# Kernel optimization log

Hardware: AMD Instinct MI355X
Metric: run time of the kernel (lower is better)

The kernel has to match this reference:

```python
import jax, jax.numpy as jnp
import numpy as np

DIM = 4096
N_HEADS = 32
HEAD_DIM = DIM // N_HEADS
BATCH = 2
SEQ = 1024
THETA = 10000.0
NEG_INF = -1e9


def _rope_cos_sin(seq_len, head_dim):
    # NOTE: original code constructs RotatePosEmbedding with config.dim but applies
    # it per-head; the only shape-consistent interpretation (standard Llama RoPE)
    # uses head_dim frequencies, which is what we implement.
    inv_freq = 1.0 / (THETA ** (jnp.arange(0, head_dim, 2, dtype=jnp.float32) / head_dim))
    angles = jnp.arange(seq_len, dtype=jnp.float32)[:, None] * inv_freq[None, :]  # [S, hd/2]
    return jnp.cos(angles), jnp.sin(angles)


def _apply_rope(x, cos, sin):
    # x: [B,S,H,hd]; rotate consecutive pairs (complex multiply)
    B, S, H, hd = x.shape
    xr = x.reshape(B, S, H, hd // 2, 2)
    x0, x1 = xr[..., 0], xr[..., 1]
    c = cos[None, :, None, :]
    s = sin[None, :, None, :]
    out = jnp.stack([x0 * c - x1 * s, x0 * s + x1 * c], axis=-1)
    return out.reshape(B, S, H, hd)


def setup_inputs() -> dict:
    key = jax.random.key(0)
    ks = jax.random.split(key, 9)
    x = jax.random.normal(ks[0], (BATCH, SEQ, DIM), dtype=jnp.float32)
    scale = 1.0 / np.sqrt(DIM)
    wq = jax.random.normal(ks[1], (DIM, DIM), dtype=jnp.float32) * scale
    wk = jax.random.normal(ks[2], (DIM, DIM), dtype=jnp.float32) * scale
    wv = jax.random.normal(ks[3], (DIM, DIM), dtype=jnp.float32) * scale
    wo = jax.random.normal(ks[4], (DIM, DIM), dtype=jnp.float32) * scale
    bq = jax.random.normal(ks[5], (DIM,), dtype=jnp.float32) * 0.01
    bk = jax.random.normal(ks[6], (DIM,), dtype=jnp.float32) * 0.01
    bv = jax.random.normal(ks[7], (DIM,), dtype=jnp.float32) * 0.01
    bo = jax.random.normal(ks[8], (DIM,), dtype=jnp.float32) * 0.01
    # causal additive mask [S,S]
    mask = jnp.where(jnp.tril(jnp.ones((SEQ, SEQ), dtype=bool)), 0.0, NEG_INF).astype(jnp.float32)
    return {"x": x, "wq": wq, "bq": bq, "wk": wk, "bk": bk, "wv": wv, "bv": bv,
            "wo": wo, "bo": bo, "mask": mask, "start_pos": 0}


def reference(x, wq, bq, wk, bk, wv, bv, wo, bo, mask, start_pos):
    B, S, D = x.shape
    H, hd = N_HEADS, D // N_HEADS
    q = (x @ wq.T + bq).reshape(B, S, H, hd)
    k = (x @ wk.T + bk).reshape(B, S, H, hd)
    v = (x @ wv.T + bv).reshape(B, S, H, hd)
    cos, sin = _rope_cos_sin(S, hd)
    q = _apply_rope(q, cos, sin)
    k = _apply_rope(k, cos, sin)
    # start_pos == 0 prefill: cache slice [:start_pos+S] equals current k/v
    scores = jnp.einsum('bqhd,bkhd->bhqk', q, k) / np.sqrt(hd).astype(np.float32)
    scores = scores + mask[None, None, :, :]
    attn = jax.nn.softmax(scores, axis=-1)
    out = jnp.einsum('bhqk,bkhd->bqhd', attn, v).reshape(B, S, D)
    return out @ wo.T + bo
```

## Files before the change

### kernel.cpp

```cpp
#include <hip/hip_runtime.h>
#include <hip/hip_bf16.h>

#define DIM   4096
#define NH    32
#define HD    128
#define BATCH 2
#define SEQ   1024
#define MROWS (BATCH*SEQ)

typedef __attribute__((ext_vector_type(8))) short bf16x8;
typedef __attribute__((ext_vector_type(4))) short s16x4;
typedef __attribute__((ext_vector_type(4))) float f32x4;

__device__ inline void gload_lds16(const void* g, void* l) {
  __builtin_amdgcn_global_load_lds(
      (const __attribute__((address_space(1))) void*)g,
      (__attribute__((address_space(3))) void*)l, 16, 0, 0);
}

__device__ inline float bf2f(short b) {
  unsigned u = ((unsigned)(unsigned short)b) << 16;
  return __uint_as_float(u);
}
__device__ inline unsigned short f2bfu(float f) {
  __hip_bfloat16 h = __float2bfloat16(f);
  return *reinterpret_cast<unsigned short*>(&h);
}

__global__ void cvt_bf16_kernel(const float* __restrict__ in,
                                unsigned short* __restrict__ out, long n4) {
  long i = blockIdx.x * (long)blockDim.x + threadIdx.x;
  long stride = (long)gridDim.x * blockDim.x;
  for (; i < n4; i += stride) {
    float4 v = ((const float4*)in)[i];
    ushort4 o;
    o.x = f2bfu(v.x); o.y = f2bfu(v.y); o.z = f2bfu(v.z); o.w = f2bfu(v.w);
    ((ushort4*)out)[i] = o;
  }
}

__global__ void rope_table_kernel(float* __restrict__ cosT, float* __restrict__ sinT) {
  int s = blockIdx.x;
  int p = threadIdx.x;
  float inv = powf(10000.0f, -((float)(2 * p)) / 128.0f);
  float a = (float)s * inv;
  cosT[s * 64 + p] = cosf(a);
  sinT[s * 64 + p] = sinf(a);
}

__global__ void rope_apply_kernel(unsigned short* __restrict__ t,
                                  const float* __restrict__ cosT,
                                  const float* __restrict__ sinT) {
  int c = blockIdx.x * blockDim.x + threadIdx.x;
  long e = (long)c * 8;
  int row = (int)(e >> 12);
  int col = (int)(e & (DIM - 1));
  int s = row & (SEQ - 1);
  int d = col & (HD - 1);
  int p0 = d >> 1;
  bf16x8 v = *(bf16x8*)&t[e];
  f32x4 cv = *(const f32x4*)&cosT[s * 64 + p0];
  f32x4 sv = *(const f32x4*)&sinT[s * 64 + p0];
  bf16x8 o;
#pragma unroll
  for (int j = 0; j < 4; ++j) {
    float x0 = bf2f(v[2 * j]);
    float x1 = bf2f(v[2 * j + 1]);
    o[2 * j]     = (short)f2bfu(x0 * cv[j] - x1 * sv[j]);
    o[2 * j + 1] = (short)f2bfu(x0 * sv[j] + x1 * cv[j]);
  }
  *(bf16x8*)&t[e] = o;
}

template <typename OutT>
__global__ __launch_bounds__(256) void gemm_bt_kernel(
    const unsigned short* __restrict__ A, const unsigned short* __restrict__ Bw,
    const float* __restrict__ bias, OutT* __restrict__ C, int M, int N, int K) {
  __shared__ unsigned short As[128 * 32];
  __shared__ unsigned short Bs[128 * 32];
  const int t = threadIdx.x;
  const int lane = t & 63;
  const int w = t >> 6;
  const int wr = w >> 1, wc = w & 1;
  const int m0 = blockIdx.y * 128;
  const int n0 = blockIdx.x * 128;

  const int ar0 = t >> 2;
  const int acol = (t & 3) * 8;
  const unsigned short* Ag0 = A + (size_t)(m0 + ar0) * K + acol;
  const unsigned short* Ag1 = A + (size_t)(m0 + 64 + ar0) * K + acol;
  const unsigned short* Bg0 = Bw + (size_t)(n0 + ar0) * K + acol;
  const unsigned short* Bg1 = Bw + (size_t)(n0 + 64 + ar0) * K + acol;
  unsigned short* Al0 = &As[(size_t)t * 8];
  unsigned short* Al1 = &As[(size_t)(256 + t) * 8];
  unsigned short* Bl0 = &Bs[(size_t)t * 8];
  unsigned short* Bl1 = &Bs[(size_t)(256 + t) * 8];

  f32x4 acc[4][4] = {};

  const int aro = wr * 64 + (lane & 15);
  const int bro = wc * 64 + (lane & 15);
  const int ko = (lane >> 4) * 8;

  for (int k0 = 0; k0 < K; k0 += 32) {
    gload_lds16(Ag0 + k0, Al0);
    gload_lds16(Ag1 + k0, Al1);
    gload_lds16(Bg0 + k0, Bl0);
    gload_lds16(Bg1 + k0, Bl1);
    __syncthreads();
    bf16x8 af[4], bfr[4];
#pragma unroll
    for (int i = 0; i < 4; ++i)
      af[i] = *(const bf16x8*)&As[(aro + i * 16) * 32 + ko];
#pragma unroll
    for (int j = 0; j < 4; ++j)
      bfr[j] = *(const bf16x8*)&Bs[(bro + j * 16) * 32 + ko];
#pragma unroll
    for (int i = 0; i < 4; ++i)
#pragma unroll
      for (int j = 0; j < 4; ++j)
        acc[i][j] = __builtin_amdgcn_mfma_f32_16x16x32_bf16(af[i], bfr[j], acc[i][j], 0, 0, 0);
    __syncthreads();
  }

  const int mrow = m0 + wr * 64 + (lane >> 4) * 4;
  const int ncol = n0 + wc * 64 + (lane & 15);
#pragma unroll
  for (int j = 0; j < 4; ++j) {
    float bj = bias[ncol + j * 16];
#pragma unroll
    for (int i = 0; i < 4; ++i) {
#pragma unroll
      for (int r = 0; r < 4; ++r) {
        float v = acc[i][j][r] + bj;
        if constexpr (sizeof(OutT) == 2) {
          ((unsigned short*)C)[(size_t)(mrow + i * 16 + r) * N + (ncol + j * 16)] = f2bfu(v);
        } else {
          ((float*)C)[(size_t)(mrow + i * 16 + r) * N + (ncol + j * 16)] = v;
        }
      }
    }
  }
}

__global__ __launch_bounds__(256, 1) void flash_attn_kernel(
    const unsigned short* __restrict__ Q, const unsigned short* __restrict__ Kk,
    const unsigned short* __restrict__ V, unsigned short* __restrict__ O) {
  __shared__ unsigned short Ks[64 * 128];
  __shared__ unsigned short Vt[128 * 64];
  __shared__ unsigned short Ps[4][32 * 64];

  const int p  = blockIdx.x;
  const int bh = blockIdx.y;
  const int b  = bh >> 5;
  const int hh = bh & 31;
  const int t    = threadIdx.x;
  const int lane = t & 63;
  const int w    = t >> 6;
  const int np   = lane & 15;
  const int hq   = lane >> 4;

  const size_t headoff = (size_t)b * SEQ * DIM + (size_t)hh * HD;
  const unsigned short* Qg = Q  + headoff;
  const unsigned short* Kg = Kk + headoff;
  const unsigned short* Vg = V  + headoff;
  unsigned short*       Og = O  + headoff;

  const int krow = t >> 2;
  const int kc0  = (t & 3) * 32;
  const int vr0  = (t & 15) * 4;
  const int vc0  = (t >> 4) * 8;

  unsigned short* Pw = &Ps[w][0];
  const float SCALE = 0.08838834764831843f;

  bf16x8 vk[4], vv[4];

#pragma unroll 1
  for (int pass = 0; pass < 2; ++pass) {
    const int qt    = pass ? (7 - p) : p;
    const int nt    = 2 * qt + 2;
    const int qbase = qt * 128 + w * 32;

    bf16x8 qf[2][4];
#pragma unroll
    for (int rb = 0; rb < 2; ++rb)
#pragma unroll
      for (int kb = 0; kb < 4; ++kb)
        qf[rb][kb] = *(const bf16x8*)&Qg[(size_t)(qbase + rb * 16 + np) * DIM + kb * 32 + hq * 8];

    f32x4 acc[2][8] = {};
    float m_run[2][4], l_run[2][4];
#pragma unroll
    for (int rb = 0; rb < 2; ++rb)
#pragma unroll
      for (int r = 0; r < 4; ++r) { m_run[rb][r] = -3.0e38f; l_run[rb][r] = 0.0f; }

    {
      const unsigned short* kp = Kg + (size_t)krow * DIM + kc0;
      const unsigned short* vp = Vg + (size_t)vr0 * DIM + vc0;
#pragma unroll
      for (int jj = 0; jj < 4; ++jj) vk[jj] = *(const bf16x8*)(kp + jj * 8);
#pragma unroll
      for (int jj = 0; jj < 4; ++jj) vv[jj] = *(const bf16x8*)(vp + (size_t)jj * DIM);
    }

#pragma unroll 1
    for (int kt = 0; kt < nt; ++kt) {
      __syncthreads();

#pragma unroll
      for (int jj = 0; jj < 4; ++jj) {
        int c = (t & 3) * 4 + jj;
        *(bf16x8*)((char*)Ks + krow * 256 + ((c ^ (krow & 7)) << 4)) = vk[jj];
      }
#pragma unroll
      for (int i = 0; i < 8; ++i) {
        int col = vc0 + i;
        s16x4 sv;
        sv[0] = vv[0][i]; sv[1] = vv[1][i]; sv[2] = vv[2][i]; sv[3] = vv[3][i];
        *(s16x4*)((char*)Vt + ((col * 128 + vr0 * 2) ^ ((col & 7) << 4))) = sv;
      }
      __syncthreads();

      if (kt + 1 < nt) {
        const unsigned short* kp = Kg + (size_t)((kt + 1) * 64 + krow) * DIM + kc0;
        const unsigned short* vp = Vg + (size_t)((kt + 1) * 64 + vr0) * DIM + vc0;
#pragma unroll
        for (int jj = 0; jj < 4; ++jj) vk[jj] = *(const bf16x8*)(kp + jj * 8);
#pragma unroll
        for (int jj = 0; jj < 4; ++jj) vv[jj] = *(const bf16x8*)(vp + (size_t)jj * DIM);
      }

      f32x4 sc[4][2] = {};
#pragma unroll
      for (int ct = 0; ct < 4; ++ct) {
#pragma unroll
        for (int kb = 0; kb < 4; ++kb) {
          bf16x8 kf = *(const bf16x8*)((char*)Ks + (ct * 16 + np) * 256 +
                                       (((kb * 4 + hq) ^ (np & 7)) << 4));
          sc[ct][0] = __builtin_amdgcn_mfma_f32_16x16x32_bf16(qf[0][kb], kf, sc[ct][0], 0, 0, 0);
          sc[ct][1] = __builtin_amdgcn_mfma_f32_16x16x32_bf16(qf[1][kb], kf, sc[ct][1], 0, 0, 0);
        }
      }

      const bool maskt = (kt >= 2 * qt);
#pragma unroll
      for (int ct = 0; ct < 4; ++ct) {
        int kvc = kt * 64 + ct * 16 + np;
#pragma unroll
        for (int rb = 0; rb < 2; ++rb)
#pragma unroll
          for (int r = 0; r < 4; ++r) {
            float v = sc[ct][rb][r] * SCALE;
            if (maskt && kvc > qbase + rb * 16 + hq * 4 + r) v = -1.0e9f;
            sc[ct][rb][r] = v;
          }
      }

      float sf[2][4];
#pragma unroll
      for (int rb = 0; rb < 2; ++rb)
#pragma unroll
        for (int r = 0; r < 4; ++r) {
          float tmax = fmaxf(fmaxf(sc[0][rb][r], sc[1][rb][r]),
                             fmaxf(sc[2][rb][r], sc[3][rb][r]));
          tmax = fmaxf(tmax, __shfl_xor(tmax, 1));
          tmax = fmaxf(tmax, __shfl_xor(tmax, 2));
          tmax = fmaxf(tmax, __shfl_xor(tmax, 4));
          tmax = fmaxf(tmax, __shfl_xor(tmax, 8));
          float mn = fmaxf(m_run[rb][r], tmax);
          sf[rb][r] = __expf(m_run[rb][r] - mn);
          m_run[rb][r] = mn;
        }

#pragma unroll
      for (int rb = 0; rb < 2; ++rb)
#pragma unroll
        for (int r = 0; r < 4; ++r) {
          int prow = rb * 16 + hq * 4 + r;
          int swz = (prow & 7) << 4;
          float rsum = 0.f;
#pragma unroll
          for (int ct = 0; ct < 4; ++ct) {
            float pv = __expf(sc[ct][rb][r] - m_run[rb][r]);
            rsum += pv;
            *(unsigned short*)((char*)Pw + ((prow * 128 + (ct * 16 + np) * 2) ^ swz)) = f2bfu(pv);
          }
          rsum += __shfl_xor(rsum, 1);
          rsum += __shfl_xor(rsum, 2);
          rsum += __shfl_xor(rsum, 4);
          rsum += __shfl_xor(rsum, 8);
          l_run[rb][r] = l_run[rb][r] * sf[rb][r] + rsum;
        }

#pragma unroll
      for (int rb = 0; rb < 2; ++rb)
#pragma unroll
        for (int nt2 = 0; nt2 < 8; ++nt2)
#pragma unroll
          for (int r = 0; r < 4; ++r)
            acc[rb][nt2][r] *= sf[rb][r];

#pragma unroll
      for (int kb2 = 0; kb2 < 2; ++kb2) {
        bf16x8 pa0 = *(const bf16x8*)((char*)Pw +
            (((0 * 16 + np) * 128 + kb2 * 64 + hq * 16) ^ ((np & 7) << 4)));
        bf16x8 pa1 = *(const bf16x8*)((char*)Pw +
            (((1 * 16 + np) * 128 + kb2 * 64 + hq * 16) ^ ((np & 7) << 4)));
#pragma unroll
        for (int nt2 = 0; nt2 < 8; ++nt2) {
          int col = nt2 * 16 + np;
          bf16x8 vf = *(const bf16x8*)((char*)Vt +
              ((col * 128 + kb2 * 64 + hq * 16) ^ ((col & 7) << 4)));
          acc[0][nt2] = __builtin_amdgcn_mfma_f32_16x16x32_bf16(pa0, vf, acc[0][nt2], 0, 0, 0);
          acc[1][nt2] = __builtin_amdgcn_mfma_f32_16x16x32_bf16(pa1, vf, acc[1][nt2], 0, 0, 0);
        }
      }
    }

#pragma unroll
    for (int rb = 0; rb < 2; ++rb)
#pragma unroll
      for (int r = 0; r < 4; ++r) {
        float rl = 1.0f / l_run[rb][r];
        int orow = qbase + rb * 16 + hq * 4 + r;
#pragma unroll
        for (int nt2 = 0; nt2 < 8; ++nt2)
          Og[(size_t)orow * DIM + nt2 * 16 + np] = f2bfu(acc[rb][nt2][r] * rl);
      }
  }
}

extern "C" void kernel_launch(void* const* d_in, const int* in_sizes, int n_in,
                              void* d_out, int out_size, void* d_ws, size_t ws_size,
                              hipStream_t stream) {
  const float* x  = (const float*)d_in[0];
  const float* wq = (const float*)d_in[1];
  const float* bq = (const float*)d_in[2];
  const float* wk = (const float*)d_in[3];
  const float* bk = (const float*)d_in[4];
  const float* wv = (const float*)d_in[5];
  const float* bv = (const float*)d_in[6];
  const float* wo = (const float*)d_in[7];
  const float* bo = (const float*)d_in[8];
  float* out = (float*)d_out;

  char* ws = (char*)d_ws;
  unsigned short* xb  = (unsigned short*)(ws);
  unsigned short* wqb = (unsigned short*)(ws + (16ll  << 20));
  unsigned short* wkb = (unsigned short*)(ws + (48ll  << 20));
  unsigned short* wvb = (unsigned short*)(ws + (80ll  << 20));
  unsigned short* wob = (unsigned short*)(ws + (112ll << 20));
  unsigned short* qb  = (unsigned short*)(ws + (144ll << 20));
  unsigned short* kb_ = (unsigned short*)(ws + (160ll << 20));
  unsigned short* vb  = (unsigned short*)(ws + (176ll << 20));
  unsigned short* ab  = (unsigned short*)(ws + (192ll << 20));
  float* cosT = (float*)(ws + (208ll << 20));
  float* sinT = (float*)(ws + (208ll << 20) + (256 << 10));

  cvt_bf16_kernel<<<2048, 256, 0, stream>>>(x,  xb,  (long)MROWS * DIM / 4);
  cvt_bf16_kernel<<<2048, 256, 0, stream>>>(wq, wqb, (long)DIM * DIM / 4);
  cvt_bf16_kernel<<<2048, 256, 0, stream>>>(wk, wkb, (long)DIM * DIM / 4);
  cvt_bf16_kernel<<<2048, 256, 0, stream>>>(wv, wvb, (long)DIM * DIM / 4);
  cvt_bf16_kernel<<<2048, 256, 0, stream>>>(wo, wob, (long)DIM * DIM / 4);

  rope_table_kernel<<<SEQ, 64, 0, stream>>>(cosT, sinT);

  dim3 gg(DIM / 128, MROWS / 128);
  gemm_bt_kernel<unsigned short><<<gg, 256, 0, stream>>>(xb, wqb, bq, qb, MROWS, DIM, DIM);
  gemm_bt_kernel<unsigned short><<<gg, 256, 0, stream>>>(xb, wkb, bk, kb_, MROWS, DIM, DIM);
  gemm_bt_kernel<unsigned short><<<gg, 256, 0, stream>>>(xb, wvb, bv, vb, MROWS, DIM, DIM);

  int rope_blocks = (MROWS * DIM / 8) / 256;
  rope_apply_kernel<<<rope_blocks, 256, 0, stream>>>(qb, cosT, sinT);
  rope_apply_kernel<<<rope_blocks, 256, 0, stream>>>(kb_, cosT, sinT);

  dim3 ga(4, BATCH * NH);
  flash_attn_kernel<<<ga, 256, 0, stream>>>(qb, kb_, vb, ab);

  gemm_bt_kernel<float><<<gg, 256, 0, stream>>>(ab, wob, bo, out, MROWS, DIM, DIM);
}
```

Baseline: 635.2 us.

## Fuse QKV projections into one GEMM with double-buffered 256x128 pipelined tiles

The Q, K and V weights are concatenated into one 12288-wide weight so a single GEMM produces a packed QKV buffer. RoPE then runs once over the Q and K columns, and flash attention reads from the packed layout with a 12288-element row stride. The GEMM kernel is rewritten to use 256x128 tiles with 512 threads, a K step of 64, double-buffered LDS loaded through XOR-swizzled direct-to-LDS copies, and a grouped block remap for cache locality. The aim is fewer launches, better reuse of x across the three projections, and overlap of global loads with MFMA work. In exchange it uses more LDS and registers per block and adds a small bias-concatenation kernel.

Measured after the change: 560.1 us. 11.8% less time.

```diff
diff --git a/kernel.cpp b/kernel.cpp
--- a/kernel.cpp
+++ b/kernel.cpp
@@ -7,6 +7,7 @@
 #define BATCH 2
 #define SEQ   1024
 #define MROWS (BATCH*SEQ)
+#define LDQ   12288
 
 typedef __attribute__((ext_vector_type(8))) short bf16x8;
 typedef __attribute__((ext_vector_type(4))) short s16x4;
@@ -39,6 +40,14 @@
   }
 }
 
+__global__ void concat3_kernel(const float* __restrict__ a, const float* __restrict__ b,
+                               const float* __restrict__ c, float* __restrict__ o) {
+  int i = blockIdx.x * blockDim.x + threadIdx.x;
+  if (i < 4096) o[i] = a[i];
+  else if (i < 8192) o[i] = b[i - 4096];
+  else if (i < 12288) o[i] = c[i - 8192];
+}
+
 __global__ void rope_table_kernel(float* __restrict__ cosT, float* __restrict__ sinT) {
   int s = blockIdx.x;
   int p = threadIdx.x;
@@ -48,17 +57,18 @@
   sinT[s * 64 + p] = sinf(a);
 }
 
-__global__ void rope_apply_kernel(unsigned short* __restrict__ t,
+__global__ void rope_apply_kernel(unsigned short* __restrict__ qkv,
                                   const float* __restrict__ cosT,
                                   const float* __restrict__ sinT) {
   int c = blockIdx.x * blockDim.x + threadIdx.x;
   long e = (long)c * 8;
-  int row = (int)(e >> 12);
-  int col = (int)(e & (DIM - 1));
+  int row = (int)(e >> 13);
+  int col = (int)(e & 8191);
   int s = row & (SEQ - 1);
   int d = col & (HD - 1);
   int p0 = d >> 1;
-  bf16x8 v = *(bf16x8*)&t[e];
+  unsigned short* p = qkv + (size_t)row * LDQ + col;
+  bf16x8 v = *(bf16x8*)p;
   f32x4 cv = *(const f32x4*)&cosT[s * 64 + p0];
   f32x4 sv = *(const f32x4*)&sinT[s * 64 + p0];
   bf16x8 o;
@@ -69,83 +79,121 @@
     o[2 * j]     = (short)f2bfu(x0 * cv[j] - x1 * sv[j]);
     o[2 * j + 1] = (short)f2bfu(x0 * sv[j] + x1 * cv[j]);
   }
-  *(bf16x8*)&t[e] = o;
+  *(bf16x8*)p = o;
+}
+
+__device__ __forceinline__ void stage_tile(
+    const unsigned short* __restrict__ A, const unsigned short* __restrict__ Bw,
+    unsigned short* Asl, unsigned short* Bsl,
+    int m0, int n0, int K, int kbase, int t) {
+#pragma unroll
+  for (int j = 0; j < 4; ++j) {
+    int ci = j * 512 + t;
+    int r = ci >> 3, c = ci & 7;
+    gload_lds16(A + (size_t)(m0 + r) * K + kbase + ((c ^ (r & 7)) << 3), Asl + ci * 8);
+  }
+#pragma unroll
+  for (int j = 0; j < 2; ++j) {
+    int ci = j * 512 + t;
+    int r = ci >> 3, c = ci & 7;
+    gload_lds16(Bw + (size_t)(n0 + r) * K + kbase + ((c ^ (r & 7)) << 3), Bsl + ci * 8);
+  }
 }
 
 template <typename OutT>
-__global__ __launch_bounds__(256) void gemm_bt_kernel(
+__global__ __launch_bounds__(512, 2) void gemm_bt_p_kernel(
     const unsigned short* __restrict__ A, const unsigned short* __restrict__ Bw,
     const float* __restrict__ bias, OutT* __restrict__ C, int M, int N, int K) {
-  __shared__ unsigned short As[128 * 32];
-  __shared__ unsigned short Bs[128 * 32];
+  __shared__ unsigned short As[2][256 * 64];
+  __shared__ unsigned short Bs[2][128 * 64];
   const int t = threadIdx.x;
   const int lane = t & 63;
   const int w = t >> 6;
-  const int wr = w >> 1, wc = w & 1;
-  const int m0 = blockIdx.y * 128;
-  const int n0 = blockIdx.x * 128;
-
-  const int ar0 = t >> 2;
-  const int acol = (t & 3) * 8;
-  const unsigned short* Ag0 = A + (size_t)(m0 + ar0) * K + acol;
-  const unsigned short* Ag1 = A + (size_t)(m0 + 64 + ar0) * K + acol;
-  const unsigned short* Bg0 = Bw + (size_t)(n0 + ar0) * K + acol;
-  const unsigned short* Bg1 = Bw + (size_t)(n0 + 64 + ar0) * K + acol;
-  unsigned short* Al0 = &As[(size_t)t * 8];
-  unsigned short* Al1 = &As[(size_t)(256 + t) * 8];
-  unsigned short* Bl0 = &Bs[(size_t)t * 8];
-  unsigned short* Bl1 = &Bs[(size_t)(256 + t) * 8];
-
-  f32x4 acc[4][4] = {};
-
-  const int aro = wr * 64 + (lane & 15);
-  const int bro = wc * 64 + (lane & 15);
-  const int ko = (lane >> 4) * 8;
-
-  for (int k0 = 0; k0 < K; k0 += 32) {
-    gload_lds16(Ag0 + k0, Al0);
-    gload_lds16(Ag1 + k0, Al1);
-    gload_lds16(Bg0 + k0, Bl0);
-    gload_lds16(Bg1 + k0, Bl1);
-    __syncthreads();
-    bf16x8 af[4], bfr[4];
-#pragma unroll
-    for (int i = 0; i < 4; ++i)
-      af[i] = *(const bf16x8*)&As[(aro + i * 16) * 32 + ko];
-#pragma unroll
-    for (int j = 0; j < 4; ++j)
-      bfr[j] = *(const bf16x8*)&Bs[(bro + j * 16) * 32 + ko];
-#pragma unroll
-    for (int i = 0; i < 4; ++i)
-#pragma unroll
-      for (int j = 0; j < 4; ++j)
-        acc[i][j] = __builtin_amdgcn_mfma_f32_16x16x32_bf16(af[i], bfr[j], acc[i][j], 0, 0, 0);
-    __syncthreads();
-  }
-
-  const int mrow = m0 + wr * 64 + (lane >> 4) * 4;
-  const int ncol = n0 + wc * 64 + (lane & 15);
-#pragma unroll
-  for (int j = 0; j < 4; ++j) {
-    float bj = bias[ncol + j * 16];
-#pragma unroll
-    for (int i = 0; i < 4; ++i) {
+  const int wm = w >> 2, wn = w & 3;
+  const int np = lane & 15, hq = lane >> 4;
+
+  int bid = blockIdx.y * gridDim.x + blockIdx.x;
+  int nwg = gridDim.x * gridDim.y;
+  int sb = (bid & 7) * (nwg >> 3) + (bid >> 3);
+  int bx = sb % gridDim.x, by = sb / gridDim.x;
+  const int m0 = by * 256, n0 = bx * 128;
+  const int NT = K >> 6;
+
+  stage_tile(A, Bw, As[0], Bs[0], m0, n0, K, 0, t);
+  stage_tile(A, Bw, As[1], Bs[1], m0, n0, K, 64, t);
+
+  f32x4 acc[8][2] = {};
+
+  asm volatile("s_waitcnt vmcnt(6)" ::: "memory");
+  __builtin_amdgcn_s_barrier();
+
+  int cur = 0;
+  for (int kt = 0; kt < NT; ++kt) {
+    const unsigned short* Asl = As[cur];
+    const unsigned short* Bsl = Bs[cur];
+    bf16x8 a0[8], b0[2];
+#pragma unroll
+    for (int i = 0; i < 8; ++i)
+      a0[i] = *(const bf16x8*)&Asl[(wm * 128 + i * 16 + np) * 64 + ((hq ^ (np & 7)) << 3)];
+#pragma unroll
+    for (int j = 0; j < 2; ++j)
+      b0[j] = *(const bf16x8*)&Bsl[(wn * 32 + j * 16 + np) * 64 + ((hq ^ (np & 7)) << 3)];
+    __builtin_amdgcn_s_setprio(1);
+#pragma unroll
+    for (int i = 0; i < 8; ++i)
+#pragma unroll
+      for (int j = 0; j < 2; ++j)
+        acc[i][j] = __builtin_amdgcn_mfma_f32_16x16x32_bf16(a0[i], b0[j], acc[i][j], 0, 0, 0);
+    __builtin_amdgcn_s_setprio(0);
+    bf16x8 a1[8], b1[2];
+#pragma unroll
+    for (int i = 0; i < 8; ++i)
+      a1[i] = *(const bf16x8*)&Asl[(wm * 128 + i * 16 + np) * 64 + (((4 + hq) ^ (np & 7)) << 3)];
+#pragma unroll
+    for (int j = 0; j < 2; ++j)
+      b1[j] = *(const bf16x8*)&Bsl[(wn * 32 + j * 16 + np) * 64 + (((4 + hq) ^ (np & 7)) << 3)];
+    asm volatile("s_waitcnt lgkmcnt(0)" ::: "memory");
+    __builtin_amdgcn_s_barrier();
+    if (kt + 2 < NT)
+      stage_tile(A, Bw, As[cur], Bs[cur], m0, n0, K, (kt + 2) << 6, t);
+    __builtin_amdgcn_s_setprio(1);
+#pragma unroll
+    for (int i = 0; i < 8; ++i)
+#pragma unroll
+      for (int j = 0; j < 2; ++j)
+        acc[i][j] = __builtin_amdgcn_mfma_f32_16x16x32_bf16(a1[i], b1[j], acc[i][j], 0, 0, 0);
+    __builtin_amdgcn_s_setprio(0);
+    if (kt + 2 < NT) {
+      asm volatile("s_waitcnt vmcnt(6)" ::: "memory");
+    } else {
+      asm volatile("s_waitcnt vmcnt(0)" ::: "memory");
+    }
+    __builtin_amdgcn_s_barrier();
+    cur ^= 1;
+  }
+
+  const int orow0 = m0 + wm * 128 + hq * 4;
+  const int ocol0 = n0 + wn * 32 + np;
+#pragma unroll
+  for (int j = 0; j < 2; ++j) {
+    float bj = bias[ocol0 + j * 16];
+#pragma unroll
+    for (int i = 0; i < 8; ++i) {
 #pragma unroll
       for (int r = 0; r < 4; ++r) {
         float v = acc[i][j][r] + bj;
-        if constexpr (sizeof(OutT) == 2) {
-          ((unsigned short*)C)[(size_t)(mrow + i * 16 + r) * N + (ncol + j * 16)] = f2bfu(v);
-        } else {
-          ((float*)C)[(size_t)(mrow + i * 16 + r) * N + (ncol + j * 16)] = v;
-        }
+        size_t off = (size_t)(orow0 + i * 16 + r) * N + (ocol0 + j * 16);
+        if constexpr (sizeof(OutT) == 2)
+          ((unsigned short*)C)[off] = f2bfu(v);
+        else
+          ((float*)C)[off] = v;
       }
     }
   }
 }
 
 __global__ __launch_bounds__(256, 1) void flash_attn_kernel(
-    const unsigned short* __restrict__ Q, const unsigned short* __restrict__ Kk,
-    const unsigned short* __restrict__ V, unsigned short* __restrict__ O) {
+    const unsigned short* __restrict__ QKV, unsigned short* __restrict__ O) {
   __shared__ unsigned short Ks[64 * 128];
   __shared__ unsigned short Vt[128 * 64];
   __shared__ unsigned short Ps[4][32 * 64];
@@ -160,11 +208,11 @@
   const int np   = lane & 15;
   const int hq   = lane >> 4;
 
-  const size_t headoff = (size_t)b * SEQ * DIM + (size_t)hh * HD;
-  const unsigned short* Qg = Q  + headoff;
-  const unsigned short* Kg = Kk + headoff;
-  const unsigned short* Vg = V  + headoff;
-  unsigned short*       Og = O  + headoff;
+  const size_t rowbase = (size_t)b * SEQ * LDQ;
+  const unsigned short* Qg = QKV + rowbase + (size_t)hh * HD;
+  const unsigned short* Kg = QKV + rowbase + 4096 + (size_t)hh * HD;
+  const unsigned short* Vg = QKV + rowbase + 8192 + (size_t)hh * HD;
+  unsigned short* Og = O + (size_t)b * SEQ * DIM + (size_t)hh * HD;
 
   const int krow = t >> 2;
   const int kc0  = (t & 3) * 32;
@@ -187,7 +235,7 @@
     for (int rb = 0; rb < 2; ++rb)
 #pragma unroll
       for (int kb = 0; kb < 4; ++kb)
-        qf[rb][kb] = *(const bf16x8*)&Qg[(size_t)(qbase + rb * 16 + np) * DIM + kb * 32 + hq * 8];
+        qf[rb][kb] = *(const bf16x8*)&Qg[(size_t)(qbase + rb * 16 + np) * LDQ + kb * 32 + hq * 8];
 
     f32x4 acc[2][8] = {};
     float m_run[2][4], l_run[2][4];
@@ -197,12 +245,12 @@
       for (int r = 0; r < 4; ++r) { m_run[rb][r] = -3.0e38f; l_run[rb][r] = 0.0f; }
 
     {
-      const unsigned short* kp = Kg + (size_t)krow * DIM + kc0;
-      const unsigned short* vp = Vg + (size_t)vr0 * DIM + vc0;
+      const unsigned short* kp = Kg + (size_t)krow * LDQ + kc0;
+      const unsigned short* vp = Vg + (size_t)vr0 * LDQ + vc0;
 #pragma unroll
       for (int jj = 0; jj < 4; ++jj) vk[jj] = *(const bf16x8*)(kp + jj * 8);
 #pragma unroll
-      for (int jj = 0; jj < 4; ++jj) vv[jj] = *(const bf16x8*)(vp + (size_t)jj * DIM);
+      for (int jj = 0; jj < 4; ++jj) vv[jj] = *(const bf16x8*)(vp + (size_t)jj * LDQ);
     }
 
 #pragma unroll 1
@@ -224,12 +272,12 @@
       __syncthreads();
 
       if (kt + 1 < nt) {
-        const unsigned short* kp = Kg + (size_t)((kt + 1) * 64 + krow) * DIM + kc0;
-        const unsigned short* vp = Vg + (size_t)((kt + 1) * 64 + vr0) * DIM + vc0;
+        const unsigned short* kp = Kg + (size_t)((kt + 1) * 64 + krow) * LDQ + kc0;
+        const unsigned short* vp = Vg + (size_t)((kt + 1) * 64 + vr0) * LDQ + vc0;
 #pragma unroll
         for (int jj = 0; jj < 4; ++jj) vk[jj] = *(const bf16x8*)(kp + jj * 8);
 #pragma unroll
-        for (int jj = 0; jj < 4; ++jj) vv[jj] = *(const bf16x8*)(vp + (size_t)jj * DIM);
+        for (int jj = 0; jj < 4; ++jj) vv[jj] = *(const bf16x8*)(vp + (size_t)jj * LDQ);
       }
 
       f32x4 sc[4][2] = {};
@@ -347,37 +395,33 @@
   float* out = (float*)d_out;
 
   char* ws = (char*)d_ws;
-  unsigned short* xb  = (unsigned short*)(ws);
-  unsigned short* wqb = (unsigned short*)(ws + (16ll  << 20));
-  unsigned short* wkb = (unsigned short*)(ws + (48ll  << 20));
-  unsigned short* wvb = (unsigned short*)(ws + (80ll  << 20));
-  unsigned short* wob = (unsigned short*)(ws + (112ll << 20));
-  unsigned short* qb  = (unsigned short*)(ws + (144ll << 20));
-  unsigned short* kb_ = (unsigned short*)(ws + (160ll << 20));
-  unsigned short* vb  = (unsigned short*)(ws + (176ll << 20));
-  unsigned short* ab  = (unsigned short*)(ws + (192ll << 20));
-  float* cosT = (float*)(ws + (208ll << 20));
-  float* sinT = (float*)(ws + (208ll << 20) + (256 << 10));
-
-  cvt_bf16_kernel<<<2048, 256, 0, stream>>>(x,  xb,  (long)MROWS * DIM / 4);
-  cvt_bf16_kernel<<<2048, 256, 0, stream>>>(wq, wqb, (long)DIM * DIM / 4);
-  cvt_bf16_kernel<<<2048, 256, 0, stream>>>(wk, wkb, (long)DIM * DIM / 4);
-  cvt_bf16_kernel<<<2048, 256, 0, stream>>>(wv, wvb, (long)DIM * DIM / 4);
+  unsigned short* wqkvb = (unsigned short*)(ws);
+  unsigned short* wob   = (unsigned short*)(ws + (96ll  << 20));
+  unsigned short* xb    = (unsigned short*)(ws + (128ll << 20));
+  unsigned short* qkv   = (unsigned short*)(ws + (144ll << 20));
+  unsigned short* ab    = (unsigned short*)(ws + (192ll << 20));
+  float* biasqkv = (float*)(ws + (208ll << 20));
+  float* cosT    = (float*)(ws + (208ll << 20) + (64  << 10));
+  float* sinT    = (float*)(ws + (208ll << 20) + (320 << 10));
+
+  cvt_bf16_kernel<<<2048, 256, 0, stream>>>(x,  xb, (long)MROWS * DIM / 4);
+  cvt_bf16_kernel<<<2048, 256, 0, stream>>>(wq, wqkvb,                       (long)DIM * DIM / 4);
+  cvt_bf16_kernel<<<2048, 256, 0, stream>>>(wk, wqkvb + (size_t)DIM * DIM,   (long)DIM * DIM / 4);
+  cvt_bf16_kernel<<<2048, 256, 0, stream>>>(wv, wqkvb + 2 * (size_t)DIM * DIM,(long)DIM * DIM / 4);
   cvt_bf16_kernel<<<2048, 256, 0, stream>>>(wo, wob, (long)DIM * DIM / 4);
 
+  concat3_kernel<<<48, 256, 0, stream>>>(bq, bk, bv, biasqkv);
   rope_table_kernel<<<SEQ, 64, 0, stream>>>(cosT, sinT);
 
-  dim3 gg(DIM / 128, MROWS / 128);
-  gemm_bt_kernel<unsigned short><<<gg, 256, 0, stream>>>(xb, wqb, bq, qb, MROWS, DIM, DIM);
-  gemm_bt_kernel<unsigned short><<<gg, 256, 0, stream>>>(xb, wkb, bk, kb_, MROWS, DIM, DIM);
-  gemm_bt_kernel<unsigned short><<<gg, 256, 0, stream>>>(xb, wvb, bv, vb, MROWS, DIM, DIM);
-
-  int rope_blocks = (MROWS * DIM / 8) / 256;
-  rope_apply_kernel<<<rope_blocks, 256, 0, stream>>>(qb, cosT, sinT);
-  rope_apply_kernel<<<rope_blocks, 256, 0, stream>>>(kb_, cosT, sinT);
+  dim3 gq(LDQ / 128, MROWS / 256);
+  gemm_bt_p_kernel<unsigned short><<<gq, 512, 0, stream>>>(xb, wqkvb, biasqkv, qkv,
+                                                           MROWS, LDQ, DIM);
+
+  rope_apply_kernel<<<(MROWS * 8192 / 8) / 256, 256, 0, stream>>>(qkv, cosT, sinT);
 
   dim3 ga(4, BATCH * NH);
-  flash_attn_kernel<<<ga, 256, 0, stream>>>(qb, kb_, vb, ab);
-
-  gemm_bt_kernel<float><<<gg, 256, 0, stream>>>(ab, wob, bo, out, MROWS, DIM, DIM);
-}
+  flash_attn_kernel<<<ga, 256, 0, stream>>>(qkv, ab);
+
+  dim3 go(DIM / 128, MROWS / 256);
+  gemm_bt_p_kernel<float><<<go, 512, 0, stream>>>(ab, wob, bo, out, MROWS, DIM, DIM);
+}
```
